# Kernel tuning notes

Measured on AMD Instinct MI355X. Metric: run time of the kernel, lower is better.

Reference implementation:

```python
import jax, jax.numpy as jnp
import numpy as np

REST = 0.0
DECAY = 0.5
THRESHOLD = 0.5
SG_WIDTH = 1.0  # rectangular surrogate-gradient window width

@jax.custom_vjp
def spike(v):
    return (v > THRESHOLD).astype(v.dtype)

def _spike_fwd(v):
    return spike(v), v

def _spike_bwd(v, g):
    # rectangular surrogate: d spike / d v = 1/width * 1[|v - threshold| < width/2]
    grad = (jnp.abs(v - THRESHOLD) < (SG_WIDTH * 0.5)).astype(g.dtype) / SG_WIDTH
    return (g * grad,)

spike.defvjp(_spike_fwd, _spike_bwd)

def setup_inputs() -> dict:
    key = jax.random.key(0)
    k1, k2, k3 = jax.random.split(key, 3)
    T, B, N = 128, 128, 1024
    tx = jax.random.normal(k1, (T, B, N), dtype=jnp.float32)
    lim = 1.0 / np.sqrt(N)  # nn.Linear default init range
    W = jax.random.uniform(k2, (N, N), dtype=jnp.float32, minval=-lim, maxval=lim)
    b = jax.random.uniform(k3, (N,), dtype=jnp.float32, minval=-lim, maxval=lim)
    return {"tx": tx, "W": W, "b": b}

def reference(tx, W, b):
    # tx: [T, B, N]; W: [N, N] (nn.Linear weight, applied as y @ W.T + b)
    v0 = jnp.full_like(tx[0], REST)
    y0 = jnp.zeros_like(tx[0])

    def step(carry, x):
        v, y = carry
        x = x + y @ W.T + b                      # recurrent input
        v = DECAY * v * (1.0 - y) + REST * y + x  # leaky integrate with reset
        y = spike(v)                              # threshold fire
        return (v, y), y

    _, ty = jax.lax.scan(step, (v0, y0), tx)
    return ty  # [T, B, N]
```

## Files before the change

### kernel.cpp

```cpp
#include <hip/hip_runtime.h>
#include <stdint.h>

#define TT 128
#define BB 128
#define NN 1024


typedef unsigned short ushort8 __attribute__((ext_vector_type(8)));

__device__ __forceinline__ float bfbits2f(uint32_t lo16) {
  union { uint32_t i; float f; } c;
  c.i = lo16 << 16;
  return c.f;
}

__global__ __launch_bounds__(256) void w_transpose_repack(
    float* __restrict__ W, uint16_t* __restrict__ WtBf,
    uint32_t* __restrict__ dirty) {
  __shared__ float ta[32][33];
  __shared__ float tb[32][33];

  int rem = blockIdx.x;
  int I = 0;
  while (rem >= (32 - I)) { rem -= (32 - I); ++I; }
  const int J = I + rem;

  const int lx = threadIdx.x & 31;
  const int ly = threadIdx.x >> 5;
  uint32_t bad = 0;

  if (I == J) {
#pragma unroll
    for (int i = 0; i < 4; ++i)
      ta[ly + i * 8][lx] = W[(I * 32 + ly + i * 8) * NN + J * 32 + lx];
    __syncthreads();
#pragma unroll
    for (int i = 0; i < 4; ++i) {
      const int idx = (I * 32 + ly + i * 8) * NN + J * 32 + lx;
      const float v = ta[lx][ly + i * 8];
      const uint32_t bits = __float_as_uint(v);
      W[idx] = v;
      WtBf[idx] = (uint16_t)(bits >> 16);
      bad |= (bits & 0xFFFFu);
    }
  } else {
#pragma unroll
    for (int i = 0; i < 4; ++i) {
      ta[ly + i * 8][lx] = W[(I * 32 + ly + i * 8) * NN + J * 32 + lx];
      tb[ly + i * 8][lx] = W[(J * 32 + ly + i * 8) * NN + I * 32 + lx];
    }
    __syncthreads();
#pragma unroll
    for (int i = 0; i < 4; ++i) {
      const int idxA = (J * 32 + ly + i * 8) * NN + I * 32 + lx;
      const float va = ta[lx][ly + i * 8];
      const uint32_t bitsA = __float_as_uint(va);
      W[idxA] = va;
      WtBf[idxA] = (uint16_t)(bitsA >> 16);
      bad |= (bitsA & 0xFFFFu);

      const int idxB = (I * 32 + ly + i * 8) * NN + J * 32 + lx;
      const float vb = tb[lx][ly + i * 8];
      const uint32_t bitsB = __float_as_uint(vb);
      W[idxB] = vb;
      WtBf[idxB] = (uint16_t)(bitsB >> 16);
      bad |= (bitsB & 0xFFFFu);
    }
  }
  const unsigned long long bm = __ballot(bad != 0);
  if ((threadIdx.x & 63) == 0 && bm) atomicOr(dirty, 1u);
}

__global__ __launch_bounds__(1024) void lif_persample(
    const void* __restrict__ tx_raw, const float* __restrict__ bias,
    const float* __restrict__ WtF32, const uint16_t* __restrict__ WtBf,
    const uint32_t* __restrict__ dirty, float* __restrict__ out) {
  const int b = blockIdx.x;
  const int tid = threadIdx.x;
  const int lane = tid & 63;
  const int wv = tid >> 6;

  __shared__ uint16_t lst[NN] __attribute__((aligned(16)));
  __shared__ int wcnt[16];
  __shared__ int sprobe;

  if (tid == 0) sprobe = 0;
  __syncthreads();
  {
    const uint32_t* txw = (const uint32_t*)tx_raw;
    int local = 0;
#pragma unroll
    for (int i = 0; i < 2; ++i) {
      const uint32_t f = (txw[tid * 2 + i] >> 7) & 0xFFu;
      local += (f >= 0x74u && f < 0x81u) ? 1 : 0;
    }
    atomicAdd(&sprobe, local);
  }
  __syncthreads();
  const bool tx_is_bf16 = (sprobe > 1024);
  const bool w_bf = (*dirty == 0u);

  const uint16_t* __restrict__ txh = (const uint16_t*)tx_raw;
  const float* __restrict__ txf = (const float*)tx_raw;
  const float bz = bias[tid];

  const int pidx = (wv < 6) ? 0 : ((wv < 12) ? 1 : 2);
  const int pw0 = (pidx == 0) ? 0 : ((pidx == 1) ? 6 : 12);

  const uint16_t* __restrict__ rowB = WtBf + tid;
  const float* __restrict__ rowF = WtF32 + tid;

  float v = 0.0f;
  int y = 0;

  auto gB = [&](int pbase, int cnt) -> float {
    float acc = 0.0f;
    for (int i = 0; i < cnt; i += 32) {
      const ushort8* lp = (const ushort8*)(lst + pbase + i);
      const ushort8 a0 = lp[0];
      const ushort8 a1 = lp[1];
      const ushort8 a2 = lp[2];
      const ushort8 a3 = lp[3];
      float wbuf[32];
#pragma unroll
      for (int u = 0; u < 8; ++u) {
        const int k = __builtin_amdgcn_readfirstlane((int)a0[u]);
        wbuf[u] = bfbits2f((uint32_t)rowB[k << 10]);
      }
#pragma unroll
      for (int u = 0; u < 8; ++u) {
        const int k = __builtin_amdgcn_readfirstlane((int)a1[u]);
        wbuf[8 + u] = bfbits2f((uint32_t)rowB[k << 10]);
      }
#pragma unroll
      for (int u = 0; u < 8; ++u) {
        const int k = __builtin_amdgcn_readfirstlane((int)a2[u]);
        wbuf[16 + u] = bfbits2f((uint32_t)rowB[k << 10]);
      }
#pragma unroll
      for (int u = 0; u < 8; ++u) {
        const int k = __builtin_amdgcn_readfirstlane((int)a3[u]);
        wbuf[24 + u] = bfbits2f((uint32_t)rowB[k << 10]);
      }
#pragma unroll
      for (int u = 0; u < 32; ++u) acc += wbuf[u];
    }
    return acc;
  };

  auto gF = [&](int s, int e) -> float {
    float acc = 0.0f;
    int i = s;
    for (; i + 8 <= e; i += 8) {
      float w[8];
#pragma unroll
      for (int u = 0; u < 8; ++u) {
        const int k = __builtin_amdgcn_readfirstlane((int)lst[i + u]);
        w[u] = rowF[k << 10];
      }
#pragma unroll
      for (int u = 0; u < 8; ++u) acc += w[u];
    }
    for (; i < e; ++i) {
      const int k = __builtin_amdgcn_readfirstlane((int)lst[i]);
      acc += rowF[k << 10];
    }
    return acc;
  };

  for (int t = 0; t < TT; ++t) {
    const unsigned long long m = __ballot(y);
    if (lane == 0) wcnt[wv] = __popcll(m);
    __syncthreads();
    int base = 0, c0 = 0, c1 = 0, c2 = 0;
#pragma unroll
    for (int w = 0; w < 16; ++w) {
      const int c = wcnt[w];
      c0 += (w < 6) ? c : 0;
      c1 += (w >= 6 && w < 12) ? c : 0;
      c2 += (w >= 12) ? c : 0;
      base += (w >= pw0 && w < wv) ? c : 0;
    }
    if (y) {
      const int below = __builtin_amdgcn_mbcnt_hi(
          (uint32_t)(m >> 32), __builtin_amdgcn_mbcnt_lo((uint32_t)m, 0));
      lst[pidx * 384 + base + below] = (uint16_t)tid;
    }
    if (tid < 96) {
      const int p = tid >> 5, j = tid & 31;
      const int c = (p == 0) ? c0 : ((p == 1) ? c1 : c2);
      if (c + j < ((c + 31) & ~31)) lst[p * 384 + c + j] = (uint16_t)NN;
    }
    __syncthreads();

    float P0, P1, P2;
    if (w_bf) {
      P0 = gB(0, (c0 + 31) & ~31);
      P1 = gB(384, (c1 + 31) & ~31);
      P2 = gB(768, (c2 + 31) & ~31);
    } else {
      P0 = gF(0, c0);
      P1 = gF(384, 384 + c1);
      P2 = gF(768, 768 + c2);
    }
    const float a = (P0 + P1) + P2;

    const int off = (t * BB + b) * NN + tid;
    const float xx = tx_is_bf16
        ? bfbits2f((uint32_t)__builtin_nontemporal_load(&txh[off]))
        : __builtin_nontemporal_load(&txf[off]);
    const float xv = (xx + a) + bz;
    v = (y ? 0.0f : 0.5f * v) + xv;
    y = (v > 0.5f);

    __builtin_nontemporal_store(y ? 1.0f : 0.0f, &out[off]);
  }
}

extern "C" void kernel_launch(void* const* d_in, const int* in_sizes, int n_in,
                              void* d_out, int out_size, void* d_ws, size_t ws_size,
                              hipStream_t stream) {
  const void* tx = nullptr;
  float* W = nullptr;
  const float* bs = nullptr;
  for (int i = 0; i < n_in; ++i) {
    if (in_sizes[i] == TT * BB * NN) tx = d_in[i];
    else if (in_sizes[i] == NN * NN) W = (float*)d_in[i];
    else if (in_sizes[i] == NN) bs = (const float*)d_in[i];
  }
  float* out = (float*)d_out;

  uint16_t* WtBf = (uint16_t*)d_ws;
  uint16_t* zrow = WtBf + NN * NN;
  uint32_t* dirty = (uint32_t*)((char*)d_ws + 2u * 1024u * 1024u + 2048u);

  hipMemsetAsync(dirty, 0, sizeof(uint32_t), stream);
  hipMemsetAsync(zrow, 0, NN * sizeof(uint16_t), stream);

  w_transpose_repack<<<dim3(528), dim3(256), 0, stream>>>(W, WtBf, dirty);
  lif_persample<<<dim3(BB), dim3(1024), 0, stream>>>(tx, bs, W, WtBf, dirty, out);
}
```

Before: 1.919 ms.

## Split each batch sample across two blocks exchanging spike masks via global flags

Each batch sample's 1024 neurons are now handled by two 512-thread blocks, giving 256 blocks instead of 128 so more of the CUs are used. Every timestep the paired blocks swap their spike ballot masks through global memory, using a release/acquire flag handshake and a 4-slot ring buffer. The tx load is issued before the barrier so its latency overlaps the sync. The cost is a cross-block spin wait each step, which can deadlock if the two blocks of a pair are not co-resident; a fallback to the old kernel is kept for when the workspace is too small.

```diff
diff --git a/kernel.cpp b/kernel.cpp
--- a/kernel.cpp
+++ b/kernel.cpp
@@ -71,17 +71,23 @@
   if ((threadIdx.x & 63) == 0 && bm) atomicOr(dirty, 1u);
 }
 
-__global__ __launch_bounds__(1024) void lif_persample(
+__global__ __launch_bounds__(512) void lif_half(
     const void* __restrict__ tx_raw, const float* __restrict__ bias,
     const float* __restrict__ WtF32, const uint16_t* __restrict__ WtBf,
-    const uint32_t* __restrict__ dirty, float* __restrict__ out) {
-  const int b = blockIdx.x;
+    const uint32_t* __restrict__ dirty,
+    unsigned long long* __restrict__ gmask, unsigned int* __restrict__ gflag,
+    float* __restrict__ out) {
+  const int bb = blockIdx.x;
+  const int b = bb & 127;
+  const int h = bb >> 7;
+  const int pp = bb ^ 128;
   const int tid = threadIdx.x;
   const int lane = tid & 63;
   const int wv = tid >> 6;
+  const int n = (h << 9) + tid;
 
   __shared__ uint16_t lst[NN] __attribute__((aligned(16)));
-  __shared__ int wcnt[16];
+  __shared__ unsigned long long smask[16];
   __shared__ int sprobe;
 
   if (tid == 0) sprobe = 0;
@@ -97,18 +103,15 @@
     atomicAdd(&sprobe, local);
   }
   __syncthreads();
-  const bool tx_is_bf16 = (sprobe > 1024);
+  const bool tx_is_bf16 = (sprobe > 512);
   const bool w_bf = (*dirty == 0u);
 
   const uint16_t* __restrict__ txh = (const uint16_t*)tx_raw;
   const float* __restrict__ txf = (const float*)tx_raw;
-  const float bz = bias[tid];
-
-  const int pidx = (wv < 6) ? 0 : ((wv < 12) ? 1 : 2);
-  const int pw0 = (pidx == 0) ? 0 : ((pidx == 1) ? 6 : 12);
-
-  const uint16_t* __restrict__ rowB = WtBf + tid;
-  const float* __restrict__ rowF = WtF32 + tid;
+  const float bz = bias[n];
+
+  const uint16_t* __restrict__ rowB = WtBf + n;
+  const float* __restrict__ rowF = WtF32 + n;
 
   float v = 0.0f;
   int y = 0;
@@ -169,6 +172,201 @@
   };
 
   for (int t = 0; t < TT; ++t) {
+    const int sl = t & 3;
+    const unsigned long long m = __ballot(y);
+    if (lane == 0) {
+      smask[h * 8 + wv] = m;
+      __hip_atomic_store(&gmask[((size_t)bb * 4 + sl) * 8 + wv], m,
+                         __ATOMIC_RELAXED, __HIP_MEMORY_SCOPE_AGENT);
+    }
+
+    const int off = (t * BB + b) * NN + n;
+    float xx;
+    if (tx_is_bf16)
+      xx = bfbits2f((uint32_t)__builtin_nontemporal_load(&txh[off]));
+    else
+      xx = __builtin_nontemporal_load(&txf[off]);
+
+    __syncthreads();
+    if (tid == 0) {
+      __threadfence();
+      __hip_atomic_store(&gflag[bb], (unsigned int)(t + 1),
+                         __ATOMIC_RELEASE, __HIP_MEMORY_SCOPE_AGENT);
+    }
+    if (tid < 8) {
+      while (__hip_atomic_load(&gflag[pp], __ATOMIC_ACQUIRE,
+                               __HIP_MEMORY_SCOPE_AGENT) < (unsigned int)(t + 1)) {
+        __builtin_amdgcn_s_sleep(1);
+      }
+      smask[(1 - h) * 8 + tid] =
+          __hip_atomic_load(&gmask[((size_t)pp * 4 + sl) * 8 + tid],
+                            __ATOMIC_RELAXED, __HIP_MEMORY_SCOPE_AGENT);
+    }
+    __syncthreads();
+
+    unsigned long long mk[16];
+    int cnt[16];
+#pragma unroll
+    for (int i = 0; i < 16; ++i) {
+      mk[i] = smask[i];
+      cnt[i] = __popcll(mk[i]);
+    }
+    int pref[16];
+    {
+      int s = 0;
+#pragma unroll
+      for (int j = 0; j < 6; ++j) { pref[j] = s; s += cnt[j]; }
+    }
+    {
+      int s = 384;
+#pragma unroll
+      for (int j = 6; j < 12; ++j) { pref[j] = s; s += cnt[j]; }
+    }
+    {
+      int s = 768;
+#pragma unroll
+      for (int j = 12; j < 16; ++j) { pref[j] = s; s += cnt[j]; }
+    }
+    const int c0 = pref[5] + cnt[5];
+    const int c1 = pref[11] + cnt[11] - 384;
+    const int c2 = pref[15] + cnt[15] - 768;
+
+#pragma unroll
+    for (int jj = 0; jj < 2; ++jj) {
+      const int j = wv * 2 + jj;
+      const unsigned long long bits = mk[j];
+      if ((bits >> lane) & 1ull) {
+        const int below = __builtin_amdgcn_mbcnt_hi(
+            (uint32_t)(bits >> 32),
+            __builtin_amdgcn_mbcnt_lo((uint32_t)bits, 0));
+        lst[pref[j] + below] = (uint16_t)(j * 64 + lane);
+      }
+    }
+    if (tid < 96) {
+      const int p = tid >> 5, jn = tid & 31;
+      const int c = (p == 0) ? c0 : ((p == 1) ? c1 : c2);
+      if (c + jn < ((c + 31) & ~31)) lst[p * 384 + c + jn] = (uint16_t)NN;
+    }
+    __syncthreads();
+
+    float P0, P1, P2;
+    if (w_bf) {
+      P0 = gB(0, (c0 + 31) & ~31);
+      P1 = gB(384, (c1 + 31) & ~31);
+      P2 = gB(768, (c2 + 31) & ~31);
+    } else {
+      P0 = gF(0, c0);
+      P1 = gF(384, 384 + c1);
+      P2 = gF(768, 768 + c2);
+    }
+    const float a = (P0 + P1) + P2;
+
+    const float xv = (xx + a) + bz;
+    v = (y ? 0.0f : 0.5f * v) + xv;
+    y = (v > 0.5f);
+
+    __builtin_nontemporal_store(y ? 1.0f : 0.0f, &out[off]);
+  }
+}
+
+__global__ __launch_bounds__(1024) void lif_persample(
+    const void* __restrict__ tx_raw, const float* __restrict__ bias,
+    const float* __restrict__ WtF32, const uint16_t* __restrict__ WtBf,
+    const uint32_t* __restrict__ dirty, float* __restrict__ out) {
+  const int b = blockIdx.x;
+  const int tid = threadIdx.x;
+  const int lane = tid & 63;
+  const int wv = tid >> 6;
+
+  __shared__ uint16_t lst[NN] __attribute__((aligned(16)));
+  __shared__ int wcnt[16];
+  __shared__ int sprobe;
+
+  if (tid == 0) sprobe = 0;
+  __syncthreads();
+  {
+    const uint32_t* txw = (const uint32_t*)tx_raw;
+    int local = 0;
+#pragma unroll
+    for (int i = 0; i < 2; ++i) {
+      const uint32_t f = (txw[tid * 2 + i] >> 7) & 0xFFu;
+      local += (f >= 0x74u && f < 0x81u) ? 1 : 0;
+    }
+    atomicAdd(&sprobe, local);
+  }
+  __syncthreads();
+  const bool tx_is_bf16 = (sprobe > 1024);
+  const bool w_bf = (*dirty == 0u);
+
+  const uint16_t* __restrict__ txh = (const uint16_t*)tx_raw;
+  const float* __restrict__ txf = (const float*)tx_raw;
+  const float bz = bias[tid];
+
+  const int pidx = (wv < 6) ? 0 : ((wv < 12) ? 1 : 2);
+  const int pw0 = (pidx == 0) ? 0 : ((pidx == 1) ? 6 : 12);
+
+  const uint16_t* __restrict__ rowB = WtBf + tid;
+  const float* __restrict__ rowF = WtF32 + tid;
+
+  float v = 0.0f;
+  int y = 0;
+
+  auto gB = [&](int pbase, int cnt) -> float {
+    float acc = 0.0f;
+    for (int i = 0; i < cnt; i += 32) {
+      const ushort8* lp = (const ushort8*)(lst + pbase + i);
+      const ushort8 a0 = lp[0];
+      const ushort8 a1 = lp[1];
+      const ushort8 a2 = lp[2];
+      const ushort8 a3 = lp[3];
+      float wbuf[32];
+#pragma unroll
+      for (int u = 0; u < 8; ++u) {
+        const int k = __builtin_amdgcn_readfirstlane((int)a0[u]);
+        wbuf[u] = bfbits2f((uint32_t)rowB[k << 10]);
+      }
+#pragma unroll
+      for (int u = 0; u < 8; ++u) {
+        const int k = __builtin_amdgcn_readfirstlane((int)a1[u]);
+        wbuf[8 + u] = bfbits2f((uint32_t)rowB[k << 10]);
+      }
+#pragma unroll
+      for (int u = 0; u < 8; ++u) {
+        const int k = __builtin_amdgcn_readfirstlane((int)a2[u]);
+        wbuf[16 + u] = bfbits2f((uint32_t)rowB[k << 10]);
+      }
+#pragma unroll
+      for (int u = 0; u < 8; ++u) {
+        const int k = __builtin_amdgcn_readfirstlane((int)a3[u]);
+        wbuf[24 + u] = bfbits2f((uint32_t)rowB[k << 10]);
+      }
+#pragma unroll
+      for (int u = 0; u < 32; ++u) acc += wbuf[u];
+    }
+    return acc;
+  };
+
+  auto gF = [&](int s, int e) -> float {
+    float acc = 0.0f;
+    int i = s;
+    for (; i + 8 <= e; i += 8) {
+      float w[8];
+#pragma unroll
+      for (int u = 0; u < 8; ++u) {
+        const int k = __builtin_amdgcn_readfirstlane((int)lst[i + u]);
+        w[u] = rowF[k << 10];
+      }
+#pragma unroll
+      for (int u = 0; u < 8; ++u) acc += w[u];
+    }
+    for (; i < e; ++i) {
+      const int k = __builtin_amdgcn_readfirstlane((int)lst[i]);
+      acc += rowF[k << 10];
+    }
+    return acc;
+  };
+
+  for (int t = 0; t < TT; ++t) {
     const unsigned long long m = __ballot(y);
     if (lane == 0) wcnt[wv] = __popcll(m);
     __syncthreads();
@@ -187,9 +385,9 @@
       lst[pidx * 384 + base + below] = (uint16_t)tid;
     }
     if (tid < 96) {
-      const int p = tid >> 5, j = tid & 31;
+      const int p = tid >> 5, jn = tid & 31;
       const int c = (p == 0) ? c0 : ((p == 1) ? c1 : c2);
-      if (c + j < ((c + 31) & ~31)) lst[p * 384 + c + j] = (uint16_t)NN;
+      if (c + jn < ((c + 31) & ~31)) lst[p * 384 + c + jn] = (uint16_t)NN;
     }
     __syncthreads();
 
@@ -230,13 +428,27 @@
   }
   float* out = (float*)d_out;
 
+  const size_t MB2 = 2u * 1024u * 1024u;
   uint16_t* WtBf = (uint16_t*)d_ws;
   uint16_t* zrow = WtBf + NN * NN;
-  uint32_t* dirty = (uint32_t*)((char*)d_ws + 2u * 1024u * 1024u + 2048u);
+  uint32_t* dirty = (uint32_t*)((char*)d_ws + MB2 + 2048u);
+  unsigned long long* gmask =
+      (unsigned long long*)((char*)d_ws + MB2 + 4096u);
+  unsigned int* gflag =
+      (unsigned int*)((char*)d_ws + MB2 + 4096u + 65536u);
+  const size_t need = MB2 + 4096u + 65536u + 1024u;
 
   hipMemsetAsync(dirty, 0, sizeof(uint32_t), stream);
   hipMemsetAsync(zrow, 0, NN * sizeof(uint16_t), stream);
 
   w_transpose_repack<<<dim3(528), dim3(256), 0, stream>>>(W, WtBf, dirty);
-  lif_persample<<<dim3(BB), dim3(1024), 0, stream>>>(tx, bs, W, WtBf, dirty, out);
+
+  if (ws_size >= need) {
+    hipMemsetAsync(gflag, 0, 256 * sizeof(unsigned int), stream);
+    lif_half<<<dim3(256), dim3(512), 0, stream>>>(tx, bs, W, WtBf, dirty,
+                                                  gmask, gflag, out);
+  } else {
+    lif_persample<<<dim3(BB), dim3(1024), 0, stream>>>(tx, bs, W, WtBf, dirty,
+                                                       out);
+  }
 }
```

Result: slower. 3.135 ms (+63.4%).
